# Kernel optimization log

Hardware: AMD Instinct MI355X
Metric: run time of the kernel (lower is better)

The kernel has to match this reference:

```python
import jax, jax.numpy as jnp
import numpy as np

HIDDEN_DIM = 128


def setup_inputs() -> dict:
    key = jax.random.key(0)
    k1, k2, k3, k4, k5 = jax.random.split(key, 5)
    B, M, N2, D = 4, 4096, 8192, 128
    return {
        "x": jax.random.normal(k1, (B, M, D), dtype=jnp.float32),
        "cond": jax.random.normal(k2, (B, N2, D), dtype=jnp.float32),
        "mask": jax.random.normal(k3, (B, M, N2 // 2), dtype=jnp.float32),
        "Wq": jax.random.normal(k4, (HIDDEN_DIM, D), dtype=jnp.float32) / np.sqrt(D),
        "Wkv": jax.random.normal(k5, (HIDDEN_DIM, D), dtype=jnp.float32) / np.sqrt(D),
    }


def reference(x, cond, mask, Wq, Wkv):
    # q: [b, m, d]; kv: [b, 2n, d] chunked along the SEQUENCE dim (dim=-2)
    q = jnp.einsum('bmi,di->bmd', x, Wq)
    kv = jnp.einsum('bni,di->bnd', cond, Wkv)
    k, v = jnp.split(kv, 2, axis=-2)          # each [b, n, d]
    scale = 1.0 / np.sqrt(HIDDEN_DIM).astype(np.float32)
    qk = jnp.einsum('bmd,bnd->bmn', q, k) * scale
    p = jax.nn.softmax(qk, axis=-1) + mask    # post-softmax mask add (as in source)
    return jnp.einsum('bmn,bnd->bmd', p, v)
```

## Files before the change

kernel.cpp:

```cpp
#include <hip/hip_runtime.h>
#include <hip/hip_bf16.h>


typedef __attribute__((ext_vector_type(8))) short bf16x8;
typedef __attribute__((ext_vector_type(4))) float f32x4;

static constexpr float kSc = 0.08838834764831845f * 1.4426950408889634f;

__device__ __forceinline__ unsigned short f2bf(float f) {
  unsigned int u = __float_as_uint(f);
  u = (u + 0x7fffu + ((u >> 16) & 1u)) >> 16;
  return (unsigned short)u;
}

__device__ __forceinline__ float fast_exp2(float v) {
#if __has_builtin(__builtin_amdgcn_exp2f)
  return __builtin_amdgcn_exp2f(v);
#else
  return exp2f(v);
#endif
}

__global__ __launch_bounds__(256) void wcvt_kernel(
    const float* __restrict__ Wq, const float* __restrict__ Wkv,
    unsigned short* __restrict__ wqb, unsigned short* __restrict__ wkb)
{
  const int t = blockIdx.x * 256 + threadIdx.x;
  #pragma unroll
  for (int s = 0; s < 2; s++) {
    const float* src = s ? Wkv : Wq;
    unsigned short* dst = s ? wkb : wqb;
    float4 a = ((const float4*)src)[t * 2], b = ((const float4*)src)[t * 2 + 1];
    ushort4 o0 = make_ushort4(f2bf(a.x), f2bf(a.y), f2bf(a.z), f2bf(a.w));
    ushort4 o1 = make_ushort4(f2bf(b.x), f2bf(b.y), f2bf(b.z), f2bf(b.w));
    ((ushort4*)dst)[t * 2] = o0;
    ((ushort4*)dst)[t * 2 + 1] = o1;
  }
}

__global__ __launch_bounds__(256) void proj_kernel(
    const float* __restrict__ x, const float* __restrict__ cond,
    const unsigned short* __restrict__ wqb, const unsigned short* __restrict__ wkb,
    unsigned short* __restrict__ qws, unsigned short* __restrict__ kws,
    unsigned short* __restrict__ vTws)
{
  __shared__ __align__(16) unsigned short lds[128 * 88];
  const int bid = blockIdx.x, tid = threadIdx.x;
  const int wave = tid >> 6, l = tid & 63, l15 = l & 15, l4 = l >> 4;

  const float* src; const unsigned short* W;
  int mode; size_t row0;
  if (bid < 256) { mode = 0; src = x; W = wqb; row0 = (size_t)bid * 64; }
  else { row0 = (size_t)(bid - 256) * 64; src = cond; W = wkb;
         mode = ((int)(row0 & 8191) < 4096) ? 1 : 2; }
  const size_t rw = row0 + wave * 16;

  f32x4 ar[8];
  const float* rp = src + (rw + l15) * 128 + l4 * 8;
  #pragma unroll
  for (int ks = 0; ks < 4; ks++) {
    ar[2 * ks]     = *(const f32x4*)(rp + ks * 32);
    ar[2 * ks + 1] = *(const f32x4*)(rp + ks * 32 + 4);
  }
  bf16x8 af[4];
  #pragma unroll
  for (int ks = 0; ks < 4; ks++) {
    bf16x8 a;
    #pragma unroll
    for (int j = 0; j < 4; j++) {
      a[j]     = (short)f2bf(ar[2 * ks][j]);
      a[4 + j] = (short)f2bf(ar[2 * ks + 1][j]);
    }
    af[ks] = a;
  }

  f32x4 acc[8];
  #pragma unroll
  for (int d = 0; d < 8; d++) acc[d] = (f32x4){0.f, 0.f, 0.f, 0.f};

  const unsigned short* wp = W + l15 * 128 + l4 * 8;
  #pragma unroll
  for (int d = 0; d < 8; d++)
    #pragma unroll
    for (int ks = 0; ks < 4; ks++) {
      bf16x8 wf = *(const bf16x8*)(wp + d * 16 * 128 + ks * 32);
      acc[d] = __builtin_amdgcn_mfma_f32_16x16x32_bf16(af[ks], wf, acc[d], 0, 0, 0);
    }

  if (mode < 2) {
    #pragma unroll
    for (int d = 0; d < 8; d++)
      #pragma unroll
      for (int r = 0; r < 4; r++)
        lds[(wave * 16 + l4 * 4 + r) * 136 + d * 16 + l15] = f2bf(acc[d][r]);
    __syncthreads();
    size_t obase; unsigned short* outp;
    if (mode == 0) { outp = qws; obase = row0; }
    else { outp = kws; obase = (row0 >> 13) * 4096 + (row0 & 8191); }
    const int row = tid >> 2, ch = (tid & 3) * 32;
    const unsigned short* sp = lds + row * 136 + ch;
    unsigned short* gp = outp + (obase + row) * 128 + ch;
    #pragma unroll
    for (int i = 0; i < 4; i++)
      *(int4*)(gp + i * 8) = *(const int4*)(sp + i * 8);
  } else {
    #pragma unroll
    for (int d = 0; d < 8; d++)
      #pragma unroll
      for (int r = 0; r < 4; r++)
        lds[(d * 16 + l15) * 88 + wave * 16 + l4 * 4 + r] = f2bf(acc[d][r]);
    __syncthreads();
    const size_t b = row0 >> 13;
    const int n0 = (int)(row0 & 8191) - 4096;
    const int dd = tid >> 1, half = tid & 1;
    const unsigned short* sp = lds + dd * 88 + half * 32;
    unsigned short* gp = vTws + ((size_t)b * 128 + dd) * 4096 + n0 + half * 32;
    #pragma unroll
    for (int i = 0; i < 4; i++)
      *(int4*)(gp + i * 8) = *(const int4*)(sp + i * 8);
  }
}

__global__ __launch_bounds__(512, 2) void attn_kernel(
    const unsigned short* __restrict__ qws,
    const unsigned short* __restrict__ kws,
    const unsigned short* __restrict__ vTws,
    const float* __restrict__ mask,
    float* __restrict__ out)
{
  __shared__ __align__(16) unsigned short pbuf[8][16][72];
  __shared__ __align__(16) float cb[64][128];
  __shared__ float stats[2][64];

  const int bid = blockIdx.x;
  const int xcd = bid & 7, grp = bid >> 3;
  const int b = xcd >> 1;
  const int m0 = (grp * 2 + (xcd & 1)) * 64;

  const int tid = threadIdx.x, w = tid >> 6, l = tid & 63;
  const int rg = w & 3, nh = w >> 2;
  const int l15 = l & 15, l4 = l >> 4;

  bf16x8 qf[4];
  {
    const unsigned short* qp = qws + ((size_t)b * 4096 + m0 + rg * 16 + l15) * 128 + l4 * 8;
    #pragma unroll
    for (int ks = 0; ks < 4; ks++) qf[ks] = *(const bf16x8*)(qp + ks * 32);
  }

  f32x4 acc1[8], acc2[8];
  #pragma unroll
  for (int d = 0; d < 8; d++) { acc1[d] = (f32x4){0,0,0,0}; acc2[d] = (f32x4){0,0,0,0}; }
  float lsum[4] = {0.f, 0.f, 0.f, 0.f};

  const unsigned short* kbase = kws  + (size_t)b * 4096 * 128 + (size_t)l15 * 128 + l4 * 8;
  const unsigned short* vbase = vTws + (size_t)b * 128 * 4096 + (size_t)l15 * 4096 + l4 * 8;
  const float* mbase = mask + ((size_t)b * 4096 + m0 + rg * 16 + l15) * 4096 + l4 * 8;

  const int nbase = nh * 2048;

  bf16x8 kf[4][4];
  #pragma unroll
  for (int ns = 0; ns < 4; ns++)
    #pragma unroll
    for (int ks = 0; ks < 4; ks++)
      kf[ns][ks] = *(const bf16x8*)(kbase + (size_t)(nbase + ns * 16) * 128 + ks * 32);
  f32x4 mreg[4];
  #pragma unroll
  for (int ks = 0; ks < 2; ks++)
    #pragma unroll
    for (int h = 0; h < 2; h++)
      mreg[ks * 2 + h] = *(const f32x4*)(mbase + nbase + ks * 32 + h * 4);

  for (int nt = 0; nt < 32; nt++) {
    const int n0 = nbase + nt * 64;
    const int nn = nbase + (nt < 31 ? nt + 1 : 31) * 64;

    bf16x8 vf[16];
    #pragma unroll
    for (int d = 0; d < 4; d++)
      #pragma unroll
      for (int ks = 0; ks < 2; ks++)
        vf[d * 2 + ks] = *(const bf16x8*)(vbase + (size_t)(d * 16) * 4096 + n0 + ks * 32);

    f32x4 sacc[4];
    #pragma unroll
    for (int ns = 0; ns < 4; ns++) {
      sacc[ns] = (f32x4){0,0,0,0};
      #pragma unroll
      for (int ks = 0; ks < 4; ks++)
        sacc[ns] = __builtin_amdgcn_mfma_f32_16x16x32_bf16(qf[ks], kf[ns][ks], sacc[ns], 0, 0, 0);
    }
    #pragma unroll
    for (int ns = 0; ns < 4; ns++)
      #pragma unroll
      for (int ks = 0; ks < 4; ks++)
        kf[ns][ks] = *(const bf16x8*)(kbase + (size_t)(nn + ns * 16) * 128 + ks * 32);

    bf16x8 a2[2];
    #pragma unroll
    for (int ks = 0; ks < 2; ks++) {
      bf16x8 t;
      #pragma unroll
      for (int j = 0; j < 4; j++) {
        t[j]     = (short)f2bf(mreg[ks * 2][j]);
        t[4 + j] = (short)f2bf(mreg[ks * 2 + 1][j]);
      }
      a2[ks] = t;
    }
    #pragma unroll
    for (int ks = 0; ks < 2; ks++)
      #pragma unroll
      for (int h = 0; h < 2; h++)
        mreg[ks * 2 + h] = *(const f32x4*)(mbase + nn + ks * 32 + h * 4);

    #pragma unroll
    for (int ns = 0; ns < 4; ns++)
      #pragma unroll
      for (int r = 0; r < 4; r++) {
        float e = fast_exp2(sacc[ns][r] * kSc);
        lsum[r] += e;
        pbuf[w][l4 * 4 + r][ns * 16 + l15] = f2bf(e);
      }

    #pragma unroll
    for (int d = 4; d < 8; d++)
      #pragma unroll
      for (int ks = 0; ks < 2; ks++)
        vf[d * 2 + ks] = *(const bf16x8*)(vbase + (size_t)(d * 16) * 4096 + n0 + ks * 32);

    bf16x8 a1[2];
    #pragma unroll
    for (int ks = 0; ks < 2; ks++)
      a1[ks] = *(const bf16x8*)&pbuf[w][l15][ks * 32 + l4 * 8];

    __builtin_amdgcn_s_setprio(1);
    #pragma unroll
    for (int d = 0; d < 8; d++)
      #pragma unroll
      for (int ks = 0; ks < 2; ks++)
        acc2[d] = __builtin_amdgcn_mfma_f32_16x16x32_bf16(a2[ks], vf[d * 2 + ks], acc2[d], 0, 0, 0);
    #pragma unroll
    for (int d = 0; d < 8; d++)
      #pragma unroll
      for (int ks = 0; ks < 2; ks++)
        acc1[d] = __builtin_amdgcn_mfma_f32_16x16x32_bf16(a1[ks], vf[d * 2 + ks], acc1[d], 0, 0, 0);
    __builtin_amdgcn_s_setprio(0);
  }

  #pragma unroll
  for (int r = 0; r < 4; r++) {
    float s = lsum[r];
    s += __shfl_xor(s, 1); s += __shfl_xor(s, 2);
    s += __shfl_xor(s, 4); s += __shfl_xor(s, 8);
    lsum[r] = s;
  }
  if (l15 == 0)
    #pragma unroll
    for (int r = 0; r < 4; r++) stats[nh][rg * 16 + l4 * 4 + r] = lsum[r];
  __syncthreads();

  float rl[4];
  #pragma unroll
  for (int r = 0; r < 4; r++)
    rl[r] = 1.0f / (stats[0][rg * 16 + l4 * 4 + r] + stats[1][rg * 16 + l4 * 4 + r]);

  if (nh == 1)
    #pragma unroll
    for (int d = 0; d < 8; d++)
      #pragma unroll
      for (int r = 0; r < 4; r++)
        cb[rg * 16 + l4 * 4 + r][d * 16 + l15] = acc1[d][r] * rl[r] + acc2[d][r];
  __syncthreads();
  if (nh == 0) {
    float* op = out + ((size_t)b * 4096 + m0) * 128;
    #pragma unroll
    for (int d = 0; d < 8; d++)
      #pragma unroll
      for (int r = 0; r < 4; r++) {
        const int row = rg * 16 + l4 * 4 + r;
        op[(size_t)row * 128 + d * 16 + l15] =
            acc1[d][r] * rl[r] + acc2[d][r] + cb[row][d * 16 + l15];
      }
  }
}

extern "C" void kernel_launch(void* const* d_in, const int* in_sizes, int n_in,
                              void* d_out, int out_size, void* d_ws, size_t ws_size,
                              hipStream_t stream) {
  const float* x    = (const float*)d_in[0];
  const float* cond = (const float*)d_in[1];
  const float* mask = (const float*)d_in[2];
  const float* Wq   = (const float*)d_in[3];
  const float* Wkv  = (const float*)d_in[4];

  unsigned short* qws = (unsigned short*)d_ws;
  unsigned short* kws = qws + (size_t)4 * 4096 * 128;
  unsigned short* vT  = kws + (size_t)4 * 4096 * 128;
  unsigned short* wqb = vT  + (size_t)4 * 128 * 4096;
  unsigned short* wkb = wqb + 128 * 128;

  hipLaunchKernelGGL(wcvt_kernel, dim3(8), dim3(256), 0, stream, Wq, Wkv, wqb, wkb);
  hipLaunchKernelGGL(proj_kernel, dim3(768), dim3(256), 0, stream,
                     x, cond, wqb, wkb, qws, kws, vT);
  hipLaunchKernelGGL(attn_kernel, dim3(256), dim3(512), 0, stream,
                     qws, kws, vT, mask, (float*)d_out);
}
```

Measured before the change: 593.3 us.

## Split attention over four N-chunks with bf16 partials and separate combine kernel

The attention kernel now runs 1024 four-wave blocks, each covering one quarter of the key sequence for 64 query rows, instead of 256 eight-wave blocks that split N in two inside the block. Each block writes packed bf16 partial accumulators and fp32 row sums to workspace, and a new combine kernel sums the four partials and normalizes. The explicit register prefetch of K, V and mask is dropped in favour of loading inside the loop, and the P buffer in LDS gets an XOR swizzle. The goal is more parallelism and occupancy. The cost is extra global traffic for the partials, an additional launch, and less precision from rounding the partial sums to bf16.

```diff
diff --git a/kernel.cpp b/kernel.cpp
--- a/kernel.cpp
+++ b/kernel.cpp
@@ -1,5 +1,4 @@
 #include <hip/hip_runtime.h>
-#include <hip/hip_bf16.h>
 
 
 typedef __attribute__((ext_vector_type(8))) short bf16x8;
@@ -31,10 +30,8 @@
     const float* src = s ? Wkv : Wq;
     unsigned short* dst = s ? wkb : wqb;
     float4 a = ((const float4*)src)[t * 2], b = ((const float4*)src)[t * 2 + 1];
-    ushort4 o0 = make_ushort4(f2bf(a.x), f2bf(a.y), f2bf(a.z), f2bf(a.w));
-    ushort4 o1 = make_ushort4(f2bf(b.x), f2bf(b.y), f2bf(b.z), f2bf(b.w));
-    ((ushort4*)dst)[t * 2] = o0;
-    ((ushort4*)dst)[t * 2 + 1] = o1;
+    ((ushort4*)dst)[t * 2]     = make_ushort4(f2bf(a.x), f2bf(a.y), f2bf(a.z), f2bf(a.w));
+    ((ushort4*)dst)[t * 2 + 1] = make_ushort4(f2bf(b.x), f2bf(b.y), f2bf(b.z), f2bf(b.w));
   }
 }
 
@@ -121,29 +118,27 @@
   }
 }
 
-__global__ __launch_bounds__(512, 2) void attn_kernel(
+__global__ __launch_bounds__(256, 3) void attn_kernel(
     const unsigned short* __restrict__ qws,
     const unsigned short* __restrict__ kws,
     const unsigned short* __restrict__ vTws,
     const float* __restrict__ mask,
-    float* __restrict__ out)
-{
-  __shared__ __align__(16) unsigned short pbuf[8][16][72];
-  __shared__ __align__(16) float cb[64][128];
-  __shared__ float stats[2][64];
+    unsigned int* __restrict__ part,
+    float* __restrict__ rsumws)
+{
+  __shared__ __align__(16) unsigned short pbuf[4][16 * 64];
 
   const int bid = blockIdx.x;
-  const int xcd = bid & 7, grp = bid >> 3;
-  const int b = xcd >> 1;
-  const int m0 = (grp * 2 + (xcd & 1)) * 64;
-
+  const int c = bid & 15, grp = bid >> 4;
+  const int b = c >> 2, ns = c & 3;
+  const int m0 = grp * 64;
   const int tid = threadIdx.x, w = tid >> 6, l = tid & 63;
-  const int rg = w & 3, nh = w >> 2;
-  const int l15 = l & 15, l4 = l >> 4;
+  const int l15 = l & 15, l4 = l >> 4, l7 = l15 & 7;
+  const int nbase = ns * 1024;
 
   bf16x8 qf[4];
   {
-    const unsigned short* qp = qws + ((size_t)b * 4096 + m0 + rg * 16 + l15) * 128 + l4 * 8;
+    const unsigned short* qp = qws + ((size_t)b * 4096 + m0 + w * 16 + l15) * 128 + l4 * 8;
     #pragma unroll
     for (int ks = 0; ks < 4; ks++) qf[ks] = *(const bf16x8*)(qp + ks * 32);
   }
@@ -153,53 +148,49 @@
   for (int d = 0; d < 8; d++) { acc1[d] = (f32x4){0,0,0,0}; acc2[d] = (f32x4){0,0,0,0}; }
   float lsum[4] = {0.f, 0.f, 0.f, 0.f};
 
-  const unsigned short* kbase = kws  + (size_t)b * 4096 * 128 + (size_t)l15 * 128 + l4 * 8;
-  const unsigned short* vbase = vTws + (size_t)b * 128 * 4096 + (size_t)l15 * 4096 + l4 * 8;
-  const float* mbase = mask + ((size_t)b * 4096 + m0 + rg * 16 + l15) * 4096 + l4 * 8;
-
-  const int nbase = nh * 2048;
-
-  bf16x8 kf[4][4];
-  #pragma unroll
-  for (int ns = 0; ns < 4; ns++)
-    #pragma unroll
-    for (int ks = 0; ks < 4; ks++)
-      kf[ns][ks] = *(const bf16x8*)(kbase + (size_t)(nbase + ns * 16) * 128 + ks * 32);
-  f32x4 mreg[4];
-  #pragma unroll
-  for (int ks = 0; ks < 2; ks++)
-    #pragma unroll
-    for (int h = 0; h < 2; h++)
-      mreg[ks * 2 + h] = *(const f32x4*)(mbase + nbase + ks * 32 + h * 4);
-
-  for (int nt = 0; nt < 32; nt++) {
-    const int n0 = nbase + nt * 64;
-    const int nn = nbase + (nt < 31 ? nt + 1 : 31) * 64;
-
-    bf16x8 vf[16];
-    #pragma unroll
-    for (int d = 0; d < 4; d++)
-      #pragma unroll
-      for (int ks = 0; ks < 2; ks++)
-        vf[d * 2 + ks] = *(const bf16x8*)(vbase + (size_t)(d * 16) * 4096 + n0 + ks * 32);
+  const unsigned short* kb = kws  + ((size_t)b * 4096 + nbase + l15) * 128 + l4 * 8;
+  const unsigned short* vb = vTws + ((size_t)b * 128 + l15) * 4096 + nbase + l4 * 8;
+  const float* mrow = mask + ((size_t)(b * 4096 + m0 + w * 16 + l15)) * 4096 + nbase + l4 * 8;
+  unsigned short* pb = &pbuf[w][0];
+
+  for (int nt = 0; nt < 16; nt++) {
+    const int n0 = nt * 64;
+
+    f32x4 mreg[4];
+    #pragma unroll
+    for (int ks = 0; ks < 2; ks++)
+      #pragma unroll
+      for (int h = 0; h < 2; h++)
+        mreg[ks * 2 + h] = *(const f32x4*)(mrow + n0 + ks * 32 + h * 4);
 
     f32x4 sacc[4];
     #pragma unroll
-    for (int ns = 0; ns < 4; ns++) {
-      sacc[ns] = (f32x4){0,0,0,0};
-      #pragma unroll
-      for (int ks = 0; ks < 4; ks++)
-        sacc[ns] = __builtin_amdgcn_mfma_f32_16x16x32_bf16(qf[ks], kf[ns][ks], sacc[ns], 0, 0, 0);
-    }
-    #pragma unroll
-    for (int ns = 0; ns < 4; ns++)
-      #pragma unroll
-      for (int ks = 0; ks < 4; ks++)
-        kf[ns][ks] = *(const bf16x8*)(kbase + (size_t)(nn + ns * 16) * 128 + ks * 32);
-
-    bf16x8 a2[2];
+    for (int nsi = 0; nsi < 4; nsi++) {
+      sacc[nsi] = (f32x4){0,0,0,0};
+      const unsigned short* kp = kb + (size_t)(n0 + nsi * 16) * 128;
+      #pragma unroll
+      for (int ks = 0; ks < 4; ks++) {
+        bf16x8 kf = *(const bf16x8*)(kp + ks * 32);
+        sacc[nsi] = __builtin_amdgcn_mfma_f32_16x16x32_bf16(qf[ks], kf, sacc[nsi], 0, 0, 0);
+      }
+    }
+
+    #pragma unroll
+    for (int nsi = 0; nsi < 4; nsi++)
+      #pragma unroll
+      for (int r = 0; r < 4; r++) {
+        float e = fast_exp2(sacc[nsi][r] * kSc);
+        lsum[r] += e;
+        const int row = l4 * 4 + r;
+        const int u2 = (nsi * 2 + (l15 >> 3)) ^ (row & 7);
+        pb[row * 64 + u2 * 8 + l7] = f2bf(e);
+      }
+
+    bf16x8 a1[2], a2[2];
     #pragma unroll
     for (int ks = 0; ks < 2; ks++) {
+      const int u2 = (ks * 4 + l4) ^ l7;
+      a1[ks] = *(const bf16x8*)&pb[l15 * 64 + u2 * 8];
       bf16x8 t;
       #pragma unroll
       for (int j = 0; j < 4; j++) {
@@ -208,43 +199,18 @@
       }
       a2[ks] = t;
     }
-    #pragma unroll
-    for (int ks = 0; ks < 2; ks++)
-      #pragma unroll
-      for (int h = 0; h < 2; h++)
-        mreg[ks * 2 + h] = *(const f32x4*)(mbase + nn + ks * 32 + h * 4);
-
-    #pragma unroll
-    for (int ns = 0; ns < 4; ns++)
-      #pragma unroll
-      for (int r = 0; r < 4; r++) {
-        float e = fast_exp2(sacc[ns][r] * kSc);
-        lsum[r] += e;
-        pbuf[w][l4 * 4 + r][ns * 16 + l15] = f2bf(e);
-      }
-
-    #pragma unroll
-    for (int d = 4; d < 8; d++)
-      #pragma unroll
-      for (int ks = 0; ks < 2; ks++)
-        vf[d * 2 + ks] = *(const bf16x8*)(vbase + (size_t)(d * 16) * 4096 + n0 + ks * 32);
-
-    bf16x8 a1[2];
-    #pragma unroll
-    for (int ks = 0; ks < 2; ks++)
-      a1[ks] = *(const bf16x8*)&pbuf[w][l15][ks * 32 + l4 * 8];
 
     __builtin_amdgcn_s_setprio(1);
     #pragma unroll
-    for (int d = 0; d < 8; d++)
-      #pragma unroll
-      for (int ks = 0; ks < 2; ks++)
-        acc2[d] = __builtin_amdgcn_mfma_f32_16x16x32_bf16(a2[ks], vf[d * 2 + ks], acc2[d], 0, 0, 0);
-    #pragma unroll
-    for (int d = 0; d < 8; d++)
-      #pragma unroll
-      for (int ks = 0; ks < 2; ks++)
-        acc1[d] = __builtin_amdgcn_mfma_f32_16x16x32_bf16(a1[ks], vf[d * 2 + ks], acc1[d], 0, 0, 0);
+    for (int d = 0; d < 8; d++) {
+      const unsigned short* vp = vb + (size_t)(d * 16) * 4096 + n0;
+      bf16x8 vf0 = *(const bf16x8*)(vp);
+      bf16x8 vf1 = *(const bf16x8*)(vp + 32);
+      acc2[d] = __builtin_amdgcn_mfma_f32_16x16x32_bf16(a2[0], vf0, acc2[d], 0, 0, 0);
+      acc2[d] = __builtin_amdgcn_mfma_f32_16x16x32_bf16(a2[1], vf1, acc2[d], 0, 0, 0);
+      acc1[d] = __builtin_amdgcn_mfma_f32_16x16x32_bf16(a1[0], vf0, acc1[d], 0, 0, 0);
+      acc1[d] = __builtin_amdgcn_mfma_f32_16x16x32_bf16(a1[1], vf1, acc1[d], 0, 0, 0);
+    }
     __builtin_amdgcn_s_setprio(0);
   }
 
@@ -257,32 +223,34 @@
   }
   if (l15 == 0)
     #pragma unroll
-    for (int r = 0; r < 4; r++) stats[nh][rg * 16 + l4 * 4 + r] = lsum[r];
-  __syncthreads();
-
-  float rl[4];
-  #pragma unroll
-  for (int r = 0; r < 4; r++)
-    rl[r] = 1.0f / (stats[0][rg * 16 + l4 * 4 + r] + stats[1][rg * 16 + l4 * 4 + r]);
-
-  if (nh == 1)
-    #pragma unroll
-    for (int d = 0; d < 8; d++)
-      #pragma unroll
-      for (int r = 0; r < 4; r++)
-        cb[rg * 16 + l4 * 4 + r][d * 16 + l15] = acc1[d][r] * rl[r] + acc2[d][r];
-  __syncthreads();
-  if (nh == 0) {
-    float* op = out + ((size_t)b * 4096 + m0) * 128;
-    #pragma unroll
-    for (int d = 0; d < 8; d++)
-      #pragma unroll
-      for (int r = 0; r < 4; r++) {
-        const int row = rg * 16 + l4 * 4 + r;
-        op[(size_t)row * 128 + d * 16 + l15] =
-            acc1[d][r] * rl[r] + acc2[d][r] + cb[row][d * 16 + l15];
-      }
-  }
+    for (int r = 0; r < 4; r++)
+      rsumws[(size_t)(ns * 4 + b) * 4096 + m0 + w * 16 + l4 * 4 + r] = lsum[r];
+
+  unsigned int* pp = part + ((size_t)(ns * 4 + b) * 4096 + m0 + w * 16) * 128;
+  #pragma unroll
+  for (int d = 0; d < 8; d++)
+    #pragma unroll
+    for (int r = 0; r < 4; r++) {
+      unsigned int u = ((unsigned int)f2bf(acc2[d][r]) << 16) | (unsigned int)f2bf(acc1[d][r]);
+      pp[(size_t)(l4 * 4 + r) * 128 + d * 16 + l15] = u;
+    }
+}
+
+__global__ __launch_bounds__(256) void combine_kernel(
+    const unsigned int* __restrict__ part, const float* __restrict__ rsumws,
+    float* __restrict__ out)
+{
+  const size_t i = (size_t)blockIdx.x * 256 + threadIdx.x;
+  const int row = (int)(i >> 7);
+  float s1 = 0.f, s2 = 0.f, rs = 0.f;
+  #pragma unroll
+  for (int ns = 0; ns < 4; ns++) {
+    unsigned int u = part[(size_t)ns * 2097152 + i];
+    s1 += __uint_as_float(u << 16);
+    s2 += __uint_as_float(u & 0xFFFF0000u);
+    rs += rsumws[ns * 16384 + row];
+  }
+  out[i] = s1 * (1.0f / rs) + s2;
 }
 
 extern "C" void kernel_launch(void* const* d_in, const int* in_sizes, int n_in,
@@ -299,10 +267,14 @@
   unsigned short* vT  = kws + (size_t)4 * 4096 * 128;
   unsigned short* wqb = vT  + (size_t)4 * 128 * 4096;
   unsigned short* wkb = wqb + 128 * 128;
+  unsigned int*  part = (unsigned int*)(wkb + 128 * 128);
+  float*         rsum = (float*)(part + (size_t)4 * 4 * 4096 * 128);
 
   hipLaunchKernelGGL(wcvt_kernel, dim3(8), dim3(256), 0, stream, Wq, Wkv, wqb, wkb);
   hipLaunchKernelGGL(proj_kernel, dim3(768), dim3(256), 0, stream,
                      x, cond, wqb, wkb, qws, kws, vT);
-  hipLaunchKernelGGL(attn_kernel, dim3(256), dim3(512), 0, stream,
-                     qws, kws, vT, mask, (float*)d_out);
-}
+  hipLaunchKernelGGL(attn_kernel, dim3(1024), dim3(256), 0, stream,
+                     qws, kws, vT, mask, part, rsum);
+  hipLaunchKernelGGL(combine_kernel, dim3(8192), dim3(256), 0, stream,
+                     part, rsum, (float*)d_out);
+}
```

Measured after the change: 701.0 us. 1.18x slower.
